# Performance work log

Hardware: AMD Instinct MI355X
Metric: run time of the kernel (lower is better)

The kernel has to match this reference:

```python
import jax, jax.numpy as jnp
import numpy as np

GRID = (8, 8)
B, C, H, W = 16, 256, 64, 64
N_NETS = GRID[0] * GRID[1]
EPS = 1e-5  # torch BatchNorm2d default


def _region_index():
    # Faithful to the original code: networks[i * j + j] == networks[j*(i+1)]
    gh, gw = GRID
    i = np.arange(gh)[:, None]
    j = np.arange(gw)[None, :]
    return (i * j + j).reshape(-1)  # [gh*gw] int indices into the 64 networks


def setup_inputs() -> dict:
    key = jax.random.key(0)
    ks = jax.random.split(key, 7)
    x = jax.random.normal(ks[0], (B, C, H, W), jnp.float32)
    gamma = 1.0 + 0.1 * jax.random.normal(ks[1], (N_NETS, C), jnp.float32)
    beta = 0.1 * jax.random.normal(ks[2], (N_NETS, C), jnp.float32)
    mean = 0.1 * jax.random.normal(ks[3], (N_NETS, C), jnp.float32)
    var = jax.random.uniform(ks[4], (N_NETS, C), jnp.float32, minval=0.5, maxval=1.5)
    conv_w = 0.05 * jax.random.normal(ks[5], (N_NETS, C, C, 3, 3), jnp.float32)
    conv_b = 0.01 * jax.random.normal(ks[6], (N_NETS, C), jnp.float32)
    return dict(x=x, gamma=gamma, beta=beta, mean=mean, var=var,
                conv_w=conv_w, conv_b=conv_b)


def reference(x, gamma, beta, mean, var, conv_w, conv_b):
    gh, gw = GRID
    b, c, h, w = x.shape
    ph, pw = h // gh, w // gw
    # [B,C,H,W] -> [gh*gw, B, C, ph, pw]
    xp = (x.reshape(b, c, gh, ph, gw, pw)
           .transpose(2, 4, 0, 1, 3, 5)
           .reshape(gh * gw, b, c, ph, pw))

    idx = jnp.asarray(_region_index())
    g, bt, m, v = gamma[idx], beta[idx], mean[idx], var[idx]
    wk, cb = conv_w[idx], conv_b[idx]

    def region(xi, gi, bi, mi, vi, wi, cbi):
        # inference-mode BatchNorm2d
        scale = (gi * jax.lax.rsqrt(vi + EPS))[None, :, None, None]
        hh = (xi - mi[None, :, None, None]) * scale + bi[None, :, None, None]
        hh = jax.nn.relu(hh)
        y = jax.lax.conv_general_dilated(
            hh, wi, window_strides=(1, 1), padding=((1, 1), (1, 1)),
            dimension_numbers=('NCHW', 'OIHW', 'NCHW'))
        return y + cbi[None, :, None, None] + xi  # residual add

    yp = jax.vmap(region)(xp, g, bt, m, v, wk, cb)  # [gh*gw, B, C, ph, pw]
    y = (yp.reshape(gh, gw, b, c, ph, pw)
           .transpose(2, 3, 0, 4, 1, 5)
           .reshape(b, c, h, w))
    return y
```

## Files before the change

### kernel.cpp

```cpp
#include <hip/hip_runtime.h>
#include <hip/hip_bf16.h>
#include <stdint.h>


typedef __attribute__((ext_vector_type(8))) short bf16x8;
typedef __attribute__((ext_vector_type(8))) unsigned short u16x8;
typedef __attribute__((ext_vector_type(4))) float f32x4;

typedef const __attribute__((address_space(1))) unsigned int gu32;
typedef __attribute__((address_space(3))) unsigned int lu32;

__device__ __forceinline__ void g2l16(const void* g, void* l) {
  __builtin_amdgcn_global_load_lds((gu32*)g, (lu32*)l, 16, 0, 0);
}

__device__ __forceinline__ unsigned short f2bf(float f) {
  return __builtin_bit_cast(unsigned short, __float2bfloat16(f));
}

__global__ __launch_bounds__(256) void wtrans_kernel(
    const float* __restrict__ w, __hip_bfloat16* __restrict__ wb) {
  const int net = blockIdx.y;
  const int co = blockIdx.x * 8 + (threadIdx.x >> 5);
  const int ci0 = (threadIdx.x & 31) * 8;

  const float* src = w + (size_t)((net * 256 + co) * 256 + ci0) * 9;
  float b[72];
#pragma unroll
  for (int i = 0; i < 18; ++i) {
    f32x4 v = ((const f32x4*)src)[i];
    b[i * 4 + 0] = v[0];
    b[i * 4 + 1] = v[1];
    b[i * 4 + 2] = v[2];
    b[i * 4 + 3] = v[3];
  }
#pragma unroll
  for (int t = 0; t < 9; ++t) {
    u16x8 o;
#pragma unroll
    for (int j = 0; j < 8; ++j) o[j] = f2bf(b[j * 9 + t]);
    *(u16x8*)(wb + (size_t)((net * 9 + t) * 256 + co) * 256 + ci0) = o;
  }
}

__global__ __launch_bounds__(256) void bnrelu_kernel(
    const float* __restrict__ x, const float* __restrict__ gamma,
    const float* __restrict__ beta, const float* __restrict__ mean,
    const float* __restrict__ var, __hip_bfloat16* __restrict__ hh) {
  const int blk = blockIdx.x;
  const int cc = blk & 3;
  const int b = (blk >> 2) & 15;
  const int reg = blk >> 6;
  const int gi = reg >> 3, gj = reg & 7;
  const int net = gj * (gi + 1);
  const int tid = threadIdx.x;
  const int c0 = cc * 64;

  __shared__ float sc[64], sh[64];
  __shared__ unsigned short tile[64 * 66];

  if (tid < 64) {
    float g = gamma[net * 256 + c0 + tid];
    float bt = beta[net * 256 + c0 + tid];
    float m = mean[net * 256 + c0 + tid];
    float v = var[net * 256 + c0 + tid];
    float s = g * rsqrtf(v + 1e-5f);
    sc[tid] = s;
    sh[tid] = bt - m * s;
  }
  __syncthreads();

  const float* xb = x + (size_t)b * (256 * 4096) + (size_t)c0 * 4096 +
                    (gi * 8) * 64 + gj * 8;
#pragma unroll
  for (int i = 0; i < 4; ++i) {
    int idx = i * 256 + tid;
    int cl = idx >> 4;
    int yy = (idx >> 1) & 7;
    int hseg = idx & 1;
    f32x4 v = *(const f32x4*)(xb + (size_t)cl * 4096 + yy * 64 + hseg * 4);
    float s = sc[cl], t0 = sh[cl];
    int pxb = yy * 8 + hseg * 4;
#pragma unroll
    for (int j = 0; j < 4; ++j) {
      float hv = fmaxf(v[j] * s + t0, 0.f);
      tile[(pxb + j) * 66 + cl] = f2bf(hv);
    }
  }
  __syncthreads();

  __hip_bfloat16* hb = hh + (size_t)(reg * 16 + b) * (64 * 256) + c0;
#pragma unroll
  for (int k = 0; k < 2; ++k) {
    int o = k * 256 + tid;
    int px = o >> 3, cg = o & 7;
    u16x8 u;
#pragma unroll
    for (int j = 0; j < 8; ++j) u[j] = tile[px * 66 + cg * 8 + j];
    *(u16x8*)(hb + px * 256 + cg * 8) = u;
  }
}

__global__ __launch_bounds__(256, 2) void conv_kernel(
    const __hip_bfloat16* __restrict__ hh,
    const __hip_bfloat16* __restrict__ wb,
    const float* __restrict__ xin,
    const float* __restrict__ cbias,
    float* __restrict__ outp) {
  __shared__ __align__(16) char sA[16384];
  __shared__ __align__(16) char sB[49152];

  const int bx = blockIdx.x;
  const int r = bx >> 4;
  const int mt = bx & 7;
  const int nt = (bx >> 3) & 1;
  const int gi = r >> 3, gj = r & 7;
  const int net = gj * (gi + 1);

  const int tid = threadIdx.x;
  const int lane = tid & 63;
  const int wv = tid >> 6;
  const int wm = (wv & 1) * 64;
  const int wn = (wv >> 1) * 64;
  const int ln = lane & 15;
  const int q = lane >> 4;

  const __hip_bfloat16* Aslab = hh + (size_t)(r * 16 + mt * 2) * (64 * 256);
  const __hip_bfloat16* Bbase =
      wb + (size_t)(net * 9) * (256 * 256) + (size_t)(nt * 128) * 256;

  int bl[4], py[4], pxr[4];
#pragma unroll
  for (int mf = 0; mf < 4; ++mf) {
    int m = wm + mf * 16 + ln;
    bl[mf] = m >> 6;
    py[mf] = (m >> 3) & 7;
    pxr[mf] = m & 7;
  }
  int boff[4][2];
#pragma unroll
  for (int nf = 0; nf < 4; ++nf) {
    int nrow = wn + nf * 16 + ln;
#pragma unroll
    for (int kk = 0; kk < 2; ++kk) {
      int sl = kk * 4 + q;
      int sp = (sl + (nrow & 7)) & 7;
      boff[nf][kk] = nrow * 128 + sp * 16;
    }
  }

  f32x4 acc[4][4];
#pragma unroll
  for (int mf = 0; mf < 4; ++mf)
#pragma unroll
    for (int nf = 0; nf < 4; ++nf)
      acc[mf][nf] = (f32x4){0.f, 0.f, 0.f, 0.f};

  const bf16x8 zero8 = {0, 0, 0, 0, 0, 0, 0, 0};

#pragma unroll 1
  for (int cc = 0; cc < 4; ++cc) {
    const int c0 = cc * 64;
#pragma unroll
    for (int i = 0; i < 4; ++i) {
      int slot = i * 256 + tid;
      int row = slot >> 3, sp = slot & 7;
      int sl = (sp - (row & 7)) & 7;
      g2l16(Aslab + (size_t)row * 256 + c0 + sl * 8, sA + slot * 16);
    }
#pragma unroll 1
    for (int g = 0; g < 3; ++g) {
#pragma unroll
      for (int tt = 0; tt < 3; ++tt) {
        const __hip_bfloat16* Btap =
            Bbase + (size_t)(g * 3 + tt) * (256 * 256);
#pragma unroll
        for (int i = 0; i < 4; ++i) {
          int slot = i * 256 + tid;
          int row = slot >> 3, sp = slot & 7;
          int sl = (sp - (row & 7)) & 7;
          g2l16(Btap + (size_t)row * 256 + c0 + sl * 8,
                sB + tt * 16384 + slot * 16);
        }
      }
      __syncthreads();

#pragma unroll
      for (int tt = 0; tt < 3; ++tt) {
        const int dy = g - 1, dx = tt - 1;
        const char* sBt = sB + tt * 16384;

        int arow[4], avalid[4];
#pragma unroll
        for (int mf = 0; mf < 4; ++mf) {
          int sy = py[mf] + dy, sx = pxr[mf] + dx;
          int v = ((unsigned)sy < 8u) & ((unsigned)sx < 8u);
          avalid[mf] = v;
          arow[mf] = (bl[mf] << 6) + (v ? (sy * 8 + sx) : 0);
        }
#pragma unroll
        for (int kk = 0; kk < 2; ++kk) {
          bf16x8 afr[4], bfr[4];
#pragma unroll
          for (int mf = 0; mf < 4; ++mf) {
            int row = arow[mf];
            int sp = ((kk * 4 + q) + (row & 7)) & 7;
            bf16x8 v = *(const bf16x8*)(sA + row * 128 + sp * 16);
            afr[mf] = avalid[mf] ? v : zero8;
          }
#pragma unroll
          for (int nf = 0; nf < 4; ++nf)
            bfr[nf] = *(const bf16x8*)(sBt + boff[nf][kk]);
#pragma unroll
          for (int mf = 0; mf < 4; ++mf)
#pragma unroll
            for (int nf = 0; nf < 4; ++nf)
              acc[mf][nf] = __builtin_amdgcn_mfma_f32_16x16x32_bf16(
                  afr[mf], bfr[nf], acc[mf][nf], 0, 0, 0);
        }
      }
      __syncthreads();
    }
  }

  const int nbase = nt * 128 + wn;
#pragma unroll
  for (int nf = 0; nf < 4; ++nf) {
    const int n = nbase + nf * 16 + ln;
    const float cb = cbias[net * 256 + n];
#pragma unroll
    for (int mf = 0; mf < 4; ++mf) {
      int mloc = wm + mf * 16 + q * 4;
      int b = mt * 2 + (mloc >> 6);
      int px = mloc & 63;
      int yy = px >> 3, x0 = px & 7;
      size_t off =
          (((size_t)b * 256 + n) * 64 + (gi * 8 + yy)) * 64 + (gj * 8 + x0);
      f32x4 res = *(const f32x4*)(xin + off);
      f32x4 o = acc[mf][nf];
      o = o + res;
      o = o + cb;
      *(f32x4*)(outp + off) = o;
    }
  }
}

extern "C" void kernel_launch(void* const* d_in, const int* in_sizes, int n_in,
                              void* d_out, int out_size, void* d_ws,
                              size_t ws_size, hipStream_t stream) {
  const float* x      = (const float*)d_in[0];
  const float* gamma  = (const float*)d_in[1];
  const float* beta   = (const float*)d_in[2];
  const float* mean   = (const float*)d_in[3];
  const float* var    = (const float*)d_in[4];
  const float* conv_w = (const float*)d_in[5];
  const float* conv_b = (const float*)d_in[6];
  float* out = (float*)d_out;

  __hip_bfloat16* wb = (__hip_bfloat16*)d_ws;
  __hip_bfloat16* hh = (__hip_bfloat16*)((char*)d_ws + 75497472);

  wtrans_kernel<<<dim3(32, 64), 256, 0, stream>>>(conv_w, wb);
  bnrelu_kernel<<<4096, 256, 0, stream>>>(x, gamma, beta, mean, var, hh);
  conv_kernel<<<1024, 256, 0, stream>>>(hh, wb, x, conv_b, out);
}
```

Baseline: 412.5 us.

## Pipeline conv weight taps through triple-buffered LDS and coalesce weight transpose

The conv kernel now streams weight taps one at a time through a three-slot LDS ring, issuing the load for tap t+2 while computing tap t, with explicit vmcnt waits and raw barriers. This replaces the load-three-then-compute grouping so global-to-LDS latency overlaps MFMA work. Block indices are also remapped so that co-resident blocks share weight tiles, and setprio is raised around the MFMA bursts. The weight transpose kernel now does coalesced f32x4 reads into an LDS staging tile before writing the bf16 layout, replacing strided per-thread reads. The A tile refill at chunk boundaries is still not overlapped, and the hand-written wait counts must stay correct.

```diff
diff --git a/kernel.cpp b/kernel.cpp
--- a/kernel.cpp
+++ b/kernel.cpp
@@ -21,25 +21,39 @@
 __global__ __launch_bounds__(256) void wtrans_kernel(
     const float* __restrict__ w, __hip_bfloat16* __restrict__ wb) {
   const int net = blockIdx.y;
-  const int co = blockIdx.x * 8 + (threadIdx.x >> 5);
-  const int ci0 = (threadIdx.x & 31) * 8;
-
-  const float* src = w + (size_t)((net * 256 + co) * 256 + ci0) * 9;
-  float b[72];
+  const int cog = blockIdx.x;
+  const int tid = threadIdx.x;
+
+  __shared__ unsigned short sw[9 * 8 * 256];
+
+  const float* src = w + (size_t)(net * 256 + cog * 8) * (256 * 9);
 #pragma unroll
   for (int i = 0; i < 18; ++i) {
-    f32x4 v = ((const f32x4*)src)[i];
-    b[i * 4 + 0] = v[0];
-    b[i * 4 + 1] = v[1];
-    b[i * 4 + 2] = v[2];
-    b[i * 4 + 3] = v[3];
-  }
+    int c4 = i * 256 + tid;
+    f32x4 v = ((const f32x4*)src)[c4];
+    int p = c4 * 4;
+#pragma unroll
+    for (int j = 0; j < 4; ++j) {
+      int pp = p + j;
+      int cos = pp / 2304;
+      int rem = pp - cos * 2304;
+      int ci = rem / 9;
+      int t = rem - ci * 9;
+      sw[(t * 8 + cos) * 256 + ci] = f2bf(v[j]);
+    }
+  }
+  __syncthreads();
+
+  __hip_bfloat16* dst =
+      wb + (size_t)(net * 9) * (256 * 256) + (size_t)(cog * 8) * 256;
+  const int e0 = tid * 8;
+  const int cos = e0 >> 8, ci0 = e0 & 255;
 #pragma unroll
   for (int t = 0; t < 9; ++t) {
-    u16x8 o;
-#pragma unroll
-    for (int j = 0; j < 8; ++j) o[j] = f2bf(b[j * 9 + t]);
-    *(u16x8*)(wb + (size_t)((net * 9 + t) * 256 + co) * 256 + ci0) = o;
+    u16x8 u;
+#pragma unroll
+    for (int j = 0; j < 8; ++j) u[j] = sw[(t * 8 + cos) * 256 + ci0 + j];
+    *(u16x8*)(dst + (size_t)t * (256 * 256) + cos * 256 + ci0) = u;
   }
 }
 
@@ -110,7 +124,8 @@
   __shared__ __align__(16) char sA[16384];
   __shared__ __align__(16) char sB[49152];
 
-  const int bx = blockIdx.x;
+  const int bxr = blockIdx.x;
+  const int bx = (bxr & 7) * 128 + (bxr >> 3);
   const int r = bx >> 4;
   const int mt = bx & 7;
   const int nt = (bx >> 3) & 1;
@@ -158,9 +173,7 @@
 
   const bf16x8 zero8 = {0, 0, 0, 0, 0, 0, 0, 0};
 
-#pragma unroll 1
-  for (int cc = 0; cc < 4; ++cc) {
-    const int c0 = cc * 64;
+  auto stageA = [&](int c0) {
 #pragma unroll
     for (int i = 0; i < 4; ++i) {
       int slot = i * 256 + tid;
@@ -168,58 +181,77 @@
       int sl = (sp - (row & 7)) & 7;
       g2l16(Aslab + (size_t)row * 256 + c0 + sl * 8, sA + slot * 16);
     }
+  };
+  auto stageB = [&](int tap, int c0, int sbuf) {
+    const __hip_bfloat16* Btap = Bbase + (size_t)tap * (256 * 256);
+#pragma unroll
+    for (int i = 0; i < 4; ++i) {
+      int slot = i * 256 + tid;
+      int row = slot >> 3, sp = slot & 7;
+      int sl = (sp - (row & 7)) & 7;
+      g2l16(Btap + (size_t)row * 256 + c0 + sl * 8,
+            sB + sbuf * 16384 + slot * 16);
+    }
+  };
+
+  stageA(0);
+  stageB(0, 0, 0);
+  stageB(1, 0, 1);
+
 #pragma unroll 1
-    for (int g = 0; g < 3; ++g) {
-#pragma unroll
-      for (int tt = 0; tt < 3; ++tt) {
-        const __hip_bfloat16* Btap =
-            Bbase + (size_t)(g * 3 + tt) * (256 * 256);
-#pragma unroll
-        for (int i = 0; i < 4; ++i) {
-          int slot = i * 256 + tid;
-          int row = slot >> 3, sp = slot & 7;
-          int sl = (sp - (row & 7)) & 7;
-          g2l16(Btap + (size_t)row * 256 + c0 + sl * 8,
-                sB + tt * 16384 + slot * 16);
+  for (int cc = 0; cc < 4; ++cc) {
+    const int c0 = cc * 64;
+#pragma unroll
+    for (int t = 0; t < 9; ++t) {
+      if (t <= 6) {
+        stageB(t + 2, c0, (t + 2) % 3);
+        asm volatile("s_waitcnt vmcnt(8)" ::: "memory");
+      } else if (t == 7) {
+        asm volatile("s_waitcnt vmcnt(4)" ::: "memory");
+      } else {
+        asm volatile("s_waitcnt vmcnt(0)" ::: "memory");
+      }
+      __builtin_amdgcn_s_barrier();
+
+      const int dy = t / 3 - 1, dx = t % 3 - 1;
+      const char* sBt = sB + (t % 3) * 16384;
+
+      int arow[4], avalid[4];
+#pragma unroll
+      for (int mf = 0; mf < 4; ++mf) {
+        int sy = py[mf] + dy, sx = pxr[mf] + dx;
+        int v = ((unsigned)sy < 8u) & ((unsigned)sx < 8u);
+        avalid[mf] = v;
+        arow[mf] = (bl[mf] << 6) + (v ? (sy * 8 + sx) : 0);
+      }
+#pragma unroll
+      for (int kk = 0; kk < 2; ++kk) {
+        bf16x8 afr[4], bfr[4];
+#pragma unroll
+        for (int mf = 0; mf < 4; ++mf) {
+          int row = arow[mf];
+          int sp = ((kk * 4 + q) + (row & 7)) & 7;
+          bf16x8 v = *(const bf16x8*)(sA + row * 128 + sp * 16);
+          afr[mf] = avalid[mf] ? v : zero8;
         }
+#pragma unroll
+        for (int nf = 0; nf < 4; ++nf)
+          bfr[nf] = *(const bf16x8*)(sBt + boff[nf][kk]);
+        __builtin_amdgcn_s_setprio(1);
+#pragma unroll
+        for (int mf = 0; mf < 4; ++mf)
+#pragma unroll
+          for (int nf = 0; nf < 4; ++nf)
+            acc[mf][nf] = __builtin_amdgcn_mfma_f32_16x16x32_bf16(
+                afr[mf], bfr[nf], acc[mf][nf], 0, 0, 0);
+        __builtin_amdgcn_s_setprio(0);
       }
-      __syncthreads();
-
-#pragma unroll
-      for (int tt = 0; tt < 3; ++tt) {
-        const int dy = g - 1, dx = tt - 1;
-        const char* sBt = sB + tt * 16384;
-
-        int arow[4], avalid[4];
-#pragma unroll
-        for (int mf = 0; mf < 4; ++mf) {
-          int sy = py[mf] + dy, sx = pxr[mf] + dx;
-          int v = ((unsigned)sy < 8u) & ((unsigned)sx < 8u);
-          avalid[mf] = v;
-          arow[mf] = (bl[mf] << 6) + (v ? (sy * 8 + sx) : 0);
-        }
-#pragma unroll
-        for (int kk = 0; kk < 2; ++kk) {
-          bf16x8 afr[4], bfr[4];
-#pragma unroll
-          for (int mf = 0; mf < 4; ++mf) {
-            int row = arow[mf];
-            int sp = ((kk * 4 + q) + (row & 7)) & 7;
-            bf16x8 v = *(const bf16x8*)(sA + row * 128 + sp * 16);
-            afr[mf] = avalid[mf] ? v : zero8;
-          }
-#pragma unroll
-          for (int nf = 0; nf < 4; ++nf)
-            bfr[nf] = *(const bf16x8*)(sBt + boff[nf][kk]);
-#pragma unroll
-          for (int mf = 0; mf < 4; ++mf)
-#pragma unroll
-            for (int nf = 0; nf < 4; ++nf)
-              acc[mf][nf] = __builtin_amdgcn_mfma_f32_16x16x32_bf16(
-                  afr[mf], bfr[nf], acc[mf][nf], 0, 0, 0);
-        }
-      }
-      __syncthreads();
+      __builtin_amdgcn_s_barrier();
+    }
+    if (cc < 3) {
+      stageA(c0 + 64);
+      stageB(0, c0 + 64, 0);
+      stageB(1, c0 + 64, 1);
     }
   }
 
```

Result: faster. 402.8 us (-2.4%).
